# Optimization experiments

Measured on AMD Instinct MI355X. Metric: run time of the kernel, lower is better.

## Reference

```python
import jax, jax.numpy as jnp
import numpy as np

# Dims: N batch, C=in=out channels, T frames, V joints, S subsets, R rel_channels, H SE hidden
N, C, T, V = 256, 64, 64, 25
S, R = 3, C // 8           # num_subset, rel_channels = in_channels // rel_reduction
O = C                       # out_channels
H = max(4, O // 4)          # SE attention_channels
BN_EPS = 1e-5


def setup_inputs() -> dict:
    key = jax.random.key(0)
    ks = jax.random.split(key, 12)
    sc = 0.1
    return {
        "x":     jax.random.normal(ks[0], (N, C, T, V), jnp.float32),
        "PA":    jax.random.normal(ks[1], (S, V, V), jnp.float32) * sc,
        "alpha": jnp.ones((S,), jnp.float32),
        # per-subset stacked 1x1-conv weights (kernel_size=1 -> plain matrices)
        "w1": jax.random.normal(ks[2], (S, R, C), jnp.float32) * (2.0 / C) ** 0.5,
        "b1": jnp.zeros((S, R), jnp.float32),
        "w2": jax.random.normal(ks[3], (S, R, C), jnp.float32) * (2.0 / C) ** 0.5,
        "b2": jnp.zeros((S, R), jnp.float32),
        "w3": jax.random.normal(ks[4], (S, O, C), jnp.float32) * (2.0 / C) ** 0.5,
        "b3": jnp.zeros((S, O), jnp.float32),
        "w4": jax.random.normal(ks[5], (S, O, R), jnp.float32) * (2.0 / R) ** 0.5,
        "b4": jnp.zeros((S, O), jnp.float32),
        # final BN (eval mode: running_mean=0, running_var=1)
        "bn_w": jnp.ones((O,), jnp.float32),
        "bn_b": jnp.zeros((O,), jnp.float32),
        # SE channel attention
        "se_w1": jax.random.normal(ks[6], (H, O), jnp.float32) * (2.0 / O) ** 0.5,
        "se_b1": jnp.zeros((H,), jnp.float32),
        "se_w2": jax.random.normal(ks[7], (O, H), jnp.float32) * (2.0 / H) ** 0.5,
        "se_b2": jnp.zeros((O,), jnp.float32),
    }


def reference(x, PA, alpha, w1, b1, w2, b2, w3, b3, w4, b4,
              bn_w, bn_b, se_w1, se_b1, se_w2, se_b2):
    # --- CTRGC for all S subsets at once ---
    # conv1(x).mean(-2) == conv1 applied to x.mean over T (1x1 conv is linear)
    xm = x.mean(axis=2)                                            # [N,C,V]
    x1 = jnp.einsum('ncv,src->nsrv', xm, w1) + b1[None, :, :, None]
    x2 = jnp.einsum('ncv,src->nsrv', xm, w2) + b2[None, :, :, None]
    x3 = jnp.einsum('nctv,soc->nsotv', x, w3) + b3[None, :, :, None, None]
    # outer-difference + tanh attention map: [N,S,R,V(u),V(v)]
    att = jnp.tanh(x1[..., :, None] - x2[..., None, :])
    m = jnp.einsum('nsruv,sor->nsouv', att, w4) + b4[None, :, :, None, None]
    Asym = PA + jnp.swapaxes(PA, -1, -2)                           # A + A^T, [S,V,V]
    m = m * alpha[None, :, None, None, None] + Asym[None, :, None, :, :]
    m = jax.nn.softmax(m, axis=-2)                                 # softmax over u (dim=-2)
    # einsum 'ncuv,nctv->nctu' per subset, summed over subsets
    y = jnp.einsum('nsouv,nsotv->notu', m, x3)                     # [N,O,T,V]
    # --- BatchNorm2d (eval: mean 0, var 1) ---
    y = y / jnp.sqrt(1.0 + BN_EPS) * bn_w[None, :, None, None] + bn_b[None, :, None, None]
    # --- SE channel attention ---
    pooled = y.mean(axis=(2, 3))                                   # [N,O]
    h = jax.nn.relu(pooled @ se_w1.T + se_b1)
    se = jax.nn.sigmoid(h @ se_w2.T + se_b2)
    y = y * se[:, :, None, None]
    # --- residual (in==out -> identity down) + ReLU ---
    return jax.nn.relu(y + x)
```

## Files before the change

### kernel.cpp

```cpp
#include <hip/hip_runtime.h>

#define NN 256
#define CC 64
#define TT 64
#define VV 25
#define SS 3
#define RR 8
#define OO 64
#define HH 16

typedef _Float16 f16;
typedef _Float16 f16x8 __attribute__((ext_vector_type(8)));
typedef float f32x4 __attribute__((ext_vector_type(4)));

#define IBN 0.9999950000374997f

#define MG_NSTRIDE 153600

__global__ __launch_bounds__(256) void kab(
    const float* __restrict__ x, const float* __restrict__ PA,
    const float* __restrict__ alpha,
    const float* __restrict__ w1, const float* __restrict__ b1,
    const float* __restrict__ w2, const float* __restrict__ b2,
    const float* __restrict__ w3, const float* __restrict__ b3,
    const float* __restrict__ w4, const float* __restrict__ b4,
    const float* __restrict__ bn_w, const float* __restrict__ bn_b,
    const float* __restrict__ se_w1, const float* __restrict__ se_b1,
    const float* __restrict__ se_w2, const float* __restrict__ se_b2,
    f16* __restrict__ m_g, float* __restrict__ se_g, f16* __restrict__ w3p_g)
{
  __shared__ float xms[CC*VV];
  __shared__ float x1s[600], x2s[600];
  __shared__ float w1s[1536], w2s[1536];
  __shared__ float asym_s[1875];
  __shared__ __attribute__((aligned(16))) float att2[625*8];
  __shared__ float xmv[CC], pooledv[OO], hbuf[HH];

  int n = blockIdx.x, tid = threadIdx.x;

  for (int i = tid; i < 1536; i += 256) { w1s[i] = w1[i]; w2s[i] = w2[i]; }
  for (int i = tid; i < 1875; i += 256) {
    int s = i / 625, rem = i - s*625, u = rem / 25, v = rem - u*25;
    asym_s[i] = PA[s*625 + u*25 + v] + PA[s*625 + v*25 + u];
  }

  {
    int c8 = tid >> 5, v = tid & 31;
    if (v < 25) {
      #pragma unroll
      for (int cp = 0; cp < 8; ++cp) {
        int c = cp*8 + c8;
        const float* p = x + (size_t)(n*CC + c)*1600 + v;
        float a = 0.f;
        #pragma unroll
        for (int t = 0; t < 64; ++t) a += p[t*25];
        xms[c*25 + v] = a * (1.0f/64.0f);
      }
    }
  }
  __syncthreads();

  for (int idx = tid; idx < 600; idx += 256) {
    int sr = idx / 25, v = idx - sr*25;
    float a1 = b1[sr], a2 = b2[sr];
    #pragma unroll
    for (int c = 0; c < 64; ++c) {
      float xv = xms[c*25 + v];
      a1 += xv * w1s[sr*64 + c];
      a2 += xv * w2s[sr*64 + c];
    }
    x1s[idx] = a1; x2s[idx] = a2;
  }

  if (tid < 64) {
    float s = 0.f;
    #pragma unroll
    for (int v = 0; v < 25; ++v) s += xms[tid*25 + v];
    xmv[tid] = s * (1.0f/25.0f);
  }
  __syncthreads();
  if (tid < 64) {
    int o = tid;
    float p = b3[o] + b3[64 + o] + b3[128 + o];
    for (int c = 0; c < 64; ++c)
      p += xmv[c] * (w3[o*64 + c] + w3[4096 + o*64 + c] + w3[8192 + o*64 + c]);
    pooledv[o] = IBN * bn_w[o] * p + bn_b[o];
  }
  __syncthreads();
  if (tid < 16) {
    float hh = se_b1[tid];
    for (int o = 0; o < 64; ++o) hh += pooledv[o] * se_w1[tid*64 + o];
    hbuf[tid] = fmaxf(hh, 0.0f);
  }
  __syncthreads();
  if (tid < 64) {
    float t = se_b2[tid];
    for (int j = 0; j < 16; ++j) t += hbuf[j] * se_w2[tid*16 + j];
    se_g[n*64 + tid] = 1.0f / (1.0f + __expf(-t));
  }

  f16* mgn = m_g + (size_t)n*MG_NSTRIDE;
  for (int s = 0; s < 3; ++s) {
    __syncthreads();
    for (int idx = tid; idx < 5000; idx += 256) {
      int uv = idx >> 3, r = idx & 7;
      int u = uv / 25, v = uv - u*25;
      att2[idx] = tanhf(x1s[(s*8 + r)*25 + u] - x2s[(s*8 + r)*25 + v]);
    }
    __syncthreads();

    float alphav = alpha[s];
    #pragma unroll
    for (int pass = 0; pass < 4; ++pass) {
      int unit = tid + pass*256;
      int ot = unit >> 5, v = unit & 31;
      int o0 = ot*2;
      if (v < 25) {
        float w4r[2][8], b4r[2];
        #pragma unroll
        for (int oo = 0; oo < 2; ++oo) {
          b4r[oo] = b4[s*64 + o0 + oo];
          #pragma unroll
          for (int r = 0; r < 8; ++r) w4r[oo][r] = w4[(s*64 + o0 + oo)*8 + r];
        }
        float acc[2][25];
        #pragma unroll
        for (int u = 0; u < 25; ++u) {
          const float* ap = &att2[(u*25 + v)*8];
          f32x4 a0 = *(const f32x4*)ap;
          f32x4 a1 = *(const f32x4*)(ap + 4);
          float asv = asym_s[s*625 + u*25 + v];
          #pragma unroll
          for (int oo = 0; oo < 2; ++oo) {
            float t = b4r[oo];
            t += a0[0]*w4r[oo][0] + a0[1]*w4r[oo][1] + a0[2]*w4r[oo][2] + a0[3]*w4r[oo][3];
            t += a1[0]*w4r[oo][4] + a1[1]*w4r[oo][5] + a1[2]*w4r[oo][6] + a1[3]*w4r[oo][7];
            acc[oo][u] = t*alphav + asv;
          }
        }
        #pragma unroll
        for (int oo = 0; oo < 2; ++oo) {
          float mx = -1e30f;
          #pragma unroll
          for (int u = 0; u < 25; ++u) mx = fmaxf(mx, acc[oo][u]);
          float sum = 0.f;
          #pragma unroll
          for (int u = 0; u < 25; ++u) {
            float e = __expf(acc[oo][u] - mx); acc[oo][u] = e; sum += e;
          }
          float inv = 1.0f / sum;
          f16* mp = mgn + (size_t)((s*64 + o0 + oo)*25)*32 + v;
          #pragma unroll
          for (int u = 0; u < 25; ++u) mp[u*32] = (f16)(acc[oo][u]*inv);
        }
      } else {
        #pragma unroll
        for (int oo = 0; oo < 2; ++oo) {
          f16* mp = mgn + (size_t)((s*64 + o0 + oo)*25)*32 + v;
          #pragma unroll
          for (int u = 0; u < 25; ++u) mp[u*32] = (f16)0.f;
        }
      }
    }
  }

  if (n == 0) {
    for (int idx = tid; idx < 12288; idx += 256) {
      int j = idx & 7, lane = (idx >> 3) & 63, kk = (idx >> 9) & 1, mi = idx >> 10;
      int s = mi >> 2, o = ((mi & 3) << 4) + (lane & 15);
      int c = kk*32 + ((lane >> 4) << 3) + j;
      w3p_g[idx] = (f16)w3[(s*64 + o)*64 + c];
    }
  }
}

struct __align__(16) SmemC {
  f16   xsT[400][72];
  f16   zs[16][16][40];
  float b3s[192];
};

__global__ __launch_bounds__(256, 2) void kc(
    const float* __restrict__ x, const float* __restrict__ b3,
    const float* __restrict__ bn_w, const float* __restrict__ bn_b,
    const f16* __restrict__ m_g, const float* __restrict__ se_g,
    const f16* __restrict__ w3p_g, float* __restrict__ out)
{
  __shared__ SmemC sm;
  int bid = blockIdx.x;
  int xcd = bid & 7, ii = bid >> 3;
  int n = xcd*32 + (ii >> 2), tt = ii & 3;
  int tid = threadIdx.x;
  int lane = tid & 63, w = tid >> 6, q = lane >> 4, l15 = lane & 15;

  {
    const float* xb = x + (size_t)n*CC*1600 + tt*400;
    #pragma unroll
    for (int it = 0; it < 50; ++it) {
      int idx = it*256 + tid;
      int cp = idx / 400, j = idx - cp*400;
      float v0 = xb[(2*cp)*1600 + j];
      float v1 = xb[(2*cp + 1)*1600 + j];
      f16* p = &sm.xsT[j][2*cp];
      p[0] = (f16)v0; p[1] = (f16)v1;
    }
    if (tid < 192) sm.b3s[tid] = b3[tid];
    for (int i = tid; i < 3840; i += 256) {
      int op = i / 240, rem = i - op*240, t = rem / 15, v = 25 + (rem - t*15);
      sm.zs[op][t][v] = (f16)0.f;
    }
  }
  __syncthreads();

  const f16x8* w3pv = (const f16x8*)w3p_g;
  const f16x8* mgv  = (const f16x8*)(m_g + (size_t)n*MG_NSTRIDE);

  for (int ob = 0; ob < 4; ++ob) {
    f32x4 yacc[4][2];
    #pragma unroll
    for (int i = 0; i < 4; ++i) {
      yacc[i][0] = (f32x4){0.f,0.f,0.f,0.f};
      yacc[i][1] = (f32x4){0.f,0.f,0.f,0.f};
    }

    for (int s = 0; s < 3; ++s) {
      f16x8 bm[4][2];
      int u2 = 16 + l15; if (u2 > 24) u2 = 24;
      #pragma unroll
      for (int i = 0; i < 4; ++i) {
        int o = ob*16 + w*4 + i;
        int rb = (s*64 + o)*25;
        bm[i][0] = mgv[(rb + l15)*4 + q];
        bm[i][1] = mgv[(rb + u2)*4 + q];
      }
      int mi = s*4 + ob;
      f16x8 a0 = w3pv[(mi*2 + 0)*64 + lane];
      f16x8 a1 = w3pv[(mi*2 + 1)*64 + lane];

      __syncthreads();

      for (int ni = w; ni < 25; ni += 4) {
        int row = ni*16 + l15;
        f16x8 bf0 = *(const f16x8*)&sm.xsT[row][q*8];
        f16x8 bf1 = *(const f16x8*)&sm.xsT[row][32 + q*8];
        f32x4 acc = (f32x4){0.f,0.f,0.f,0.f};
        acc = __builtin_amdgcn_mfma_f32_16x16x32_f16(a0, bf0, acc, 0, 0, 0);
        acc = __builtin_amdgcn_mfma_f32_16x16x32_f16(a1, bf1, acc, 0, 0, 0);
        int t = row / 25, v = row - t*25;
        #pragma unroll
        for (int rg = 0; rg < 4; ++rg) {
          int op = q*4 + rg;
          sm.zs[op][t][v] = (f16)(acc[rg] + sm.b3s[s*64 + ob*16 + op]);
        }
      }
      __syncthreads();

      #pragma unroll
      for (int i = 0; i < 4; ++i) {
        int op = w*4 + i;
        f16x8 az = *(const f16x8*)&sm.zs[op][l15][q*8];
        yacc[i][0] = __builtin_amdgcn_mfma_f32_16x16x32_f16(az, bm[i][0], yacc[i][0], 0, 0, 0);
        yacc[i][1] = __builtin_amdgcn_mfma_f32_16x16x32_f16(az, bm[i][1], yacc[i][1], 0, 0, 0);
      }
    }

    #pragma unroll
    for (int i = 0; i < 4; ++i) {
      int op = w*4 + i, o = ob*16 + op;
      float sev   = se_g[n*64 + o];
      float scale = IBN * bn_w[o] * sev;
      float bias  = bn_b[o] * sev;
      #pragma unroll
      for (int ut = 0; ut < 2; ++ut) {
        int u = ut*16 + l15;
        if (u < 25) {
          #pragma unroll
          for (int rg = 0; rg < 4; ++rg) {
            int t = q*4 + rg;
            float xres = (float)sm.xsT[t*25 + u][o];
            float val = yacc[i][ut][rg]*scale + bias + xres;
            out[(((size_t)n*64 + o)*64 + tt*16 + t)*25 + u] = fmaxf(val, 0.0f);
          }
        }
      }
    }
  }
}

extern "C" void kernel_launch(void* const* d_in, const int* in_sizes, int n_in,
                              void* d_out, int out_size, void* d_ws, size_t ws_size,
                              hipStream_t stream)
{
  const float* x    = (const float*)d_in[0];
  const float* PA   = (const float*)d_in[1];
  const float* alp  = (const float*)d_in[2];
  const float* w1   = (const float*)d_in[3];
  const float* b1   = (const float*)d_in[4];
  const float* w2   = (const float*)d_in[5];
  const float* b2   = (const float*)d_in[6];
  const float* w3   = (const float*)d_in[7];
  const float* b3   = (const float*)d_in[8];
  const float* w4   = (const float*)d_in[9];
  const float* b4   = (const float*)d_in[10];
  const float* bnw  = (const float*)d_in[11];
  const float* bnb  = (const float*)d_in[12];
  const float* sw1  = (const float*)d_in[13];
  const float* sb1  = (const float*)d_in[14];
  const float* sw2  = (const float*)d_in[15];
  const float* sb2  = (const float*)d_in[16];

  char* ws = (char*)d_ws;
  f16*   m_g   = (f16*)ws;
  float* se_g  = (float*)(ws + 78643200);
  f16*   w3p_g = (f16*)(ws + 78643200 + 65536);

  float* out = (float*)d_out;

  kab<<<256, 256, 0, stream>>>(x, PA, alp, w1, b1, w2, b2, w3, b3, w4, b4,
                               bnw, bnb, sw1, sb1, sw2, sb2, m_g, se_g, w3p_g);
  kc<<<1024, 256, 0, stream>>>(x, b3, bnw, bnb, m_g, se_g, w3p_g, out);
}
```

Measured before the change: 344.2 us.

## Split attention-map kernel into mean-pool and per-subset softmax kernels

Result: slower. 356.5 us (+3.6%).

```diff
diff --git a/kernel.cpp b/kernel.cpp
--- a/kernel.cpp
+++ b/kernel.cpp
@@ -17,60 +17,51 @@
 
 #define MG_NSTRIDE 153600
 
-__global__ __launch_bounds__(256) void kab(
-    const float* __restrict__ x, const float* __restrict__ PA,
-    const float* __restrict__ alpha,
-    const float* __restrict__ w1, const float* __restrict__ b1,
-    const float* __restrict__ w2, const float* __restrict__ b2,
+__device__ __forceinline__ float tanh_fast(float xx) {
+  float e = __expf(2.0f * xx);
+  return 1.0f - __fdividef(2.0f, e + 1.0f);
+}
+
+__global__ __launch_bounds__(256) void ka(
+    const float* __restrict__ x,
     const float* __restrict__ w3, const float* __restrict__ b3,
-    const float* __restrict__ w4, const float* __restrict__ b4,
     const float* __restrict__ bn_w, const float* __restrict__ bn_b,
     const float* __restrict__ se_w1, const float* __restrict__ se_b1,
     const float* __restrict__ se_w2, const float* __restrict__ se_b2,
-    f16* __restrict__ m_g, float* __restrict__ se_g, f16* __restrict__ w3p_g)
+    float* __restrict__ xm_g, float* __restrict__ se_g,
+    f16* __restrict__ w3p_g)
 {
-  __shared__ float xms[CC*VV];
-  __shared__ float x1s[600], x2s[600];
-  __shared__ float w1s[1536], w2s[1536];
-  __shared__ float asym_s[1875];
-  __shared__ __attribute__((aligned(16))) float att2[625*8];
-  __shared__ float xmv[CC], pooledv[OO], hbuf[HH];
+  __shared__ float part[64][4][25];
+  __shared__ float xms[1600];
+  __shared__ float xmv[64], pooledv[64], hbuf[16];
 
   int n = blockIdx.x, tid = threadIdx.x;
-
-  for (int i = tid; i < 1536; i += 256) { w1s[i] = w1[i]; w2s[i] = w2[i]; }
-  for (int i = tid; i < 1875; i += 256) {
-    int s = i / 625, rem = i - s*625, u = rem / 25, v = rem - u*25;
-    asym_s[i] = PA[s*625 + u*25 + v] + PA[s*625 + v*25 + u];
-  }
-
-  {
-    int c8 = tid >> 5, v = tid & 31;
-    if (v < 25) {
-      #pragma unroll
-      for (int cp = 0; cp < 8; ++cp) {
-        int c = cp*8 + c8;
-        const float* p = x + (size_t)(n*CC + c)*1600 + v;
-        float a = 0.f;
-        #pragma unroll
-        for (int t = 0; t < 64; ++t) a += p[t*25];
-        xms[c*25 + v] = a * (1.0f/64.0f);
-      }
-    }
-  }
-  __syncthreads();
-
-  for (int idx = tid; idx < 600; idx += 256) {
-    int sr = idx / 25, v = idx - sr*25;
-    float a1 = b1[sr], a2 = b2[sr];
-    #pragma unroll
-    for (int c = 0; c < 64; ++c) {
-      float xv = xms[c*25 + v];
-      a1 += xv * w1s[sr*64 + c];
-      a2 += xv * w2s[sr*64 + c];
-    }
-    x1s[idx] = a1; x2s[idx] = a2;
-  }
+  int c = tid >> 2, tq = tid & 3;
+
+  const float* p = x + (size_t)(n*64 + c)*1600 + tq*400;
+  float acc[25];
+  #pragma unroll
+  for (int i = 0; i < 25; ++i) acc[i] = 0.f;
+  #pragma unroll
+  for (int j = 0; j < 100; ++j) {
+    f32x4 vv = *(const f32x4*)(p + 4*j);
+    acc[(4*j + 0) % 25] += vv[0];
+    acc[(4*j + 1) % 25] += vv[1];
+    acc[(4*j + 2) % 25] += vv[2];
+    acc[(4*j + 3) % 25] += vv[3];
+  }
+  #pragma unroll
+  for (int i = 0; i < 25; ++i) part[c][tq][i] = acc[i];
+  __syncthreads();
+
+  for (int idx = tid; idx < 1600; idx += 256) {
+    int cc = idx / 25, v = idx - cc*25;
+    float s = (part[cc][0][v] + part[cc][1][v] + part[cc][2][v] + part[cc][3][v])
+              * (1.0f/64.0f);
+    xms[idx] = s;
+    xm_g[n*1600 + idx] = s;
+  }
+  __syncthreads();
 
   if (tid < 64) {
     float s = 0.f;
@@ -81,10 +72,10 @@
   __syncthreads();
   if (tid < 64) {
     int o = tid;
-    float p = b3[o] + b3[64 + o] + b3[128 + o];
-    for (int c = 0; c < 64; ++c)
-      p += xmv[c] * (w3[o*64 + c] + w3[4096 + o*64 + c] + w3[8192 + o*64 + c]);
-    pooledv[o] = IBN * bn_w[o] * p + bn_b[o];
+    float pp = b3[o] + b3[64 + o] + b3[128 + o];
+    for (int cc = 0; cc < 64; ++cc)
+      pp += xmv[cc] * (w3[o*64 + cc] + w3[4096 + o*64 + cc] + w3[8192 + o*64 + cc]);
+    pooledv[o] = IBN * bn_w[o] * pp + bn_b[o];
   }
   __syncthreads();
   if (tid < 16) {
@@ -99,78 +90,125 @@
     se_g[n*64 + tid] = 1.0f / (1.0f + __expf(-t));
   }
 
-  f16* mgn = m_g + (size_t)n*MG_NSTRIDE;
-  for (int s = 0; s < 3; ++s) {
-    __syncthreads();
-    for (int idx = tid; idx < 5000; idx += 256) {
-      int uv = idx >> 3, r = idx & 7;
-      int u = uv / 25, v = uv - u*25;
-      att2[idx] = tanhf(x1s[(s*8 + r)*25 + u] - x2s[(s*8 + r)*25 + v]);
-    }
-    __syncthreads();
-
-    float alphav = alpha[s];
-    #pragma unroll
-    for (int pass = 0; pass < 4; ++pass) {
-      int unit = tid + pass*256;
-      int ot = unit >> 5, v = unit & 31;
-      int o0 = ot*2;
-      if (v < 25) {
-        float w4r[2][8], b4r[2];
-        #pragma unroll
-        for (int oo = 0; oo < 2; ++oo) {
-          b4r[oo] = b4[s*64 + o0 + oo];
-          #pragma unroll
-          for (int r = 0; r < 8; ++r) w4r[oo][r] = w4[(s*64 + o0 + oo)*8 + r];
-        }
-        float acc[2][25];
-        #pragma unroll
-        for (int u = 0; u < 25; ++u) {
-          const float* ap = &att2[(u*25 + v)*8];
-          f32x4 a0 = *(const f32x4*)ap;
-          f32x4 a1 = *(const f32x4*)(ap + 4);
-          float asv = asym_s[s*625 + u*25 + v];
-          #pragma unroll
-          for (int oo = 0; oo < 2; ++oo) {
-            float t = b4r[oo];
-            t += a0[0]*w4r[oo][0] + a0[1]*w4r[oo][1] + a0[2]*w4r[oo][2] + a0[3]*w4r[oo][3];
-            t += a1[0]*w4r[oo][4] + a1[1]*w4r[oo][5] + a1[2]*w4r[oo][6] + a1[3]*w4r[oo][7];
-            acc[oo][u] = t*alphav + asv;
-          }
-        }
-        #pragma unroll
-        for (int oo = 0; oo < 2; ++oo) {
-          float mx = -1e30f;
-          #pragma unroll
-          for (int u = 0; u < 25; ++u) mx = fmaxf(mx, acc[oo][u]);
-          float sum = 0.f;
-          #pragma unroll
-          for (int u = 0; u < 25; ++u) {
-            float e = __expf(acc[oo][u] - mx); acc[oo][u] = e; sum += e;
-          }
-          float inv = 1.0f / sum;
-          f16* mp = mgn + (size_t)((s*64 + o0 + oo)*25)*32 + v;
-          #pragma unroll
-          for (int u = 0; u < 25; ++u) mp[u*32] = (f16)(acc[oo][u]*inv);
-        }
-      } else {
-        #pragma unroll
-        for (int oo = 0; oo < 2; ++oo) {
-          f16* mp = mgn + (size_t)((s*64 + o0 + oo)*25)*32 + v;
-          #pragma unroll
-          for (int u = 0; u < 25; ++u) mp[u*32] = (f16)0.f;
-        }
-      }
-    }
-  }
-
   if (n == 0) {
     for (int idx = tid; idx < 12288; idx += 256) {
       int j = idx & 7, lane = (idx >> 3) & 63, kk = (idx >> 9) & 1, mi = idx >> 10;
       int s = mi >> 2, o = ((mi & 3) << 4) + (lane & 15);
-      int c = kk*32 + ((lane >> 4) << 3) + j;
-      w3p_g[idx] = (f16)w3[(s*64 + o)*64 + c];
-    }
+      int cc = kk*32 + ((lane >> 4) << 3) + j;
+      w3p_g[idx] = (f16)w3[(s*64 + o)*64 + cc];
+    }
+  }
+}
+
+__global__ __launch_bounds__(256, 2) void kb(
+    const float* __restrict__ xm_g, const float* __restrict__ PA,
+    const float* __restrict__ alpha,
+    const float* __restrict__ w1, const float* __restrict__ b1,
+    const float* __restrict__ w2, const float* __restrict__ b2,
+    const float* __restrict__ w4, const float* __restrict__ b4,
+    f16* __restrict__ m_g)
+{
+  __shared__ float xms[1600];
+  __shared__ float x1s[200], x2s[200];
+  __shared__ float w1s[512], w2s[512];
+  __shared__ float asym_s[625];
+  __shared__ __attribute__((aligned(16))) float att2[5000];
+  __shared__ __attribute__((aligned(16))) f16 mt[16][25][32];
+
+  int bid = blockIdx.x;
+  int n = bid & 255, s = bid >> 8;
+  int tid = threadIdx.x;
+
+  {
+    const f32x4* src = (const f32x4*)(xm_g + n*1600);
+    f32x4* dst = (f32x4*)xms;
+    for (int i = tid; i < 400; i += 256) dst[i] = src[i];
+  }
+  for (int i = tid; i < 512; i += 256) {
+    w1s[i] = w1[s*512 + i];
+    w2s[i] = w2[s*512 + i];
+  }
+  for (int i = tid; i < 625; i += 256) {
+    int u = i / 25, v = i - u*25;
+    asym_s[i] = PA[s*625 + i] + PA[s*625 + v*25 + u];
+  }
+  for (int i = tid; i < 2800; i += 256) {
+    int o = i / 175, rem = i - o*175, u = rem / 7, k = rem - u*7;
+    mt[o][u][25 + k] = (f16)0.f;
+  }
+  __syncthreads();
+
+  if (tid < 200) {
+    int r = tid / 25, v = tid - r*25;
+    float a1 = b1[s*8 + r], a2 = b2[s*8 + r];
+    #pragma unroll
+    for (int c = 0; c < 64; ++c) {
+      float xv = xms[c*25 + v];
+      a1 += xv * w1s[r*64 + c];
+      a2 += xv * w2s[r*64 + c];
+    }
+    x1s[tid] = a1; x2s[tid] = a2;
+  }
+  __syncthreads();
+
+  for (int idx = tid; idx < 5000; idx += 256) {
+    int uv = idx >> 3, r = idx & 7;
+    int u = uv / 25, v = uv - u*25;
+    att2[idx] = tanh_fast(x1s[r*25 + u] - x2s[r*25 + v]);
+  }
+  __syncthreads();
+
+  float alphav = alpha[s];
+  f16x8* mg8 = (f16x8*)(m_g + (size_t)n*MG_NSTRIDE);
+
+  for (int oq = 0; oq < 4; ++oq) {
+    if (tid < 200) {
+      int ot = tid / 25, v = tid - ot*25;
+      int o0 = oq*16 + ot*2;
+      float w4r[2][8], b4r[2];
+      #pragma unroll
+      for (int oo = 0; oo < 2; ++oo) {
+        b4r[oo] = b4[s*64 + o0 + oo];
+        #pragma unroll
+        for (int r = 0; r < 8; ++r) w4r[oo][r] = w4[(s*64 + o0 + oo)*8 + r];
+      }
+      float acc[2][25];
+      #pragma unroll
+      for (int u = 0; u < 25; ++u) {
+        const float* ap = &att2[(u*25 + v)*8];
+        f32x4 a0 = *(const f32x4*)ap;
+        f32x4 a1 = *(const f32x4*)(ap + 4);
+        float asv = asym_s[u*25 + v];
+        #pragma unroll
+        for (int oo = 0; oo < 2; ++oo) {
+          float t = b4r[oo];
+          t += a0[0]*w4r[oo][0] + a0[1]*w4r[oo][1] + a0[2]*w4r[oo][2] + a0[3]*w4r[oo][3];
+          t += a1[0]*w4r[oo][4] + a1[1]*w4r[oo][5] + a1[2]*w4r[oo][6] + a1[3]*w4r[oo][7];
+          acc[oo][u] = t*alphav + asv;
+        }
+      }
+      #pragma unroll
+      for (int oo = 0; oo < 2; ++oo) {
+        float mx = -1e30f;
+        #pragma unroll
+        for (int u = 0; u < 25; ++u) mx = fmaxf(mx, acc[oo][u]);
+        float sum = 0.f;
+        #pragma unroll
+        for (int u = 0; u < 25; ++u) {
+          float e = __expf(acc[oo][u] - mx); acc[oo][u] = e; sum += e;
+        }
+        float inv = 1.0f / sum;
+        #pragma unroll
+        for (int u = 0; u < 25; ++u) mt[ot*2 + oo][u][v] = (f16)(acc[oo][u]*inv);
+      }
+    }
+    __syncthreads();
+    for (int idx = tid; idx < 1600; idx += 256) {
+      int ol = idx / 100, rem = idx - ol*100, u = rem >> 2, vc = rem & 3;
+      int o = oq*16 + ol;
+      mg8[((size_t)(s*64 + o)*25 + u)*4 + vc] = *(const f16x8*)&mt[ol][u][vc*8];
+    }
+    __syncthreads();
   }
 }
 
@@ -313,10 +351,12 @@
   f16*   m_g   = (f16*)ws;
   float* se_g  = (float*)(ws + 78643200);
   f16*   w3p_g = (f16*)(ws + 78643200 + 65536);
+  float* xm_g  = (float*)(ws + 78643200 + 65536 + 24576);
 
   float* out = (float*)d_out;
 
-  kab<<<256, 256, 0, stream>>>(x, PA, alp, w1, b1, w2, b2, w3, b3, w4, b4,
-                               bnw, bnb, sw1, sb1, sw2, sb2, m_g, se_g, w3p_g);
+  ka<<<256, 256, 0, stream>>>(x, w3, b3, bnw, bnb, sw1, sb1, sw2, sb2,
+                              xm_g, se_g, w3p_g);
+  kb<<<768, 256, 0, stream>>>(xm_g, PA, alp, w1, b1, w2, b2, w4, b4, m_g);
   kc<<<1024, 256, 0, stream>>>(x, b3, bnw, bnb, m_g, se_g, w3p_g, out);
 }
```
